# Performance work log

Measured on AMD Instinct MI355X. Metric: run time of the kernel, lower is better.

The kernel has to match this reference:

```python
import jax, jax.numpy as jnp
import numpy as np
from jax.scipy.special import logsumexp

# Special-tag indices (module-level globals in the original repo)
PAD_IDX, SOS_IDX, EOS_IDX = 0, 1, 2
NEG = -10000.0


def setup_inputs() -> dict:
    L, B, T = 1024, 2048, 16
    key = jax.random.key(0)
    k1, k2, k3, k4 = jax.random.split(key, 4)
    h = jax.random.normal(k1, (L, B, T), dtype=jnp.float32)
    y0 = jax.random.randint(k2, (L + 1, B), 0, T)  # gold tag path, [L+1, B]
    # prefix-of-ones mask from random lengths in [L//2, L]
    lengths = jax.random.randint(k4, (B,), L // 2, L + 1)
    mask = (jnp.arange(L)[:, None] < lengths[None, :]).astype(jnp.float32)
    # transition matrix, init as in CRF.__init__
    trans = jax.random.normal(k3, (T, T), dtype=jnp.float32) * 0.01
    trans = (trans.at[SOS_IDX, :].set(NEG)
                  .at[:, EOS_IDX].set(NEG)
                  .at[:, PAD_IDX].set(NEG)
                  .at[PAD_IDX, :].set(NEG)
                  .at[PAD_IDX, EOS_IDX].set(0.0)
                  .at[PAD_IDX, PAD_IDX].set(0.0))
    return {"h": h, "y0": y0, "mask": mask, "trans": trans}


def _crf_loss(h, y0, mask, trans):
    L, B, T = h.shape
    # ---- score(h, y0, mask): note original uses _emit = 0 (emissions unused here)
    # S[b] = sum_t trans[y0[t+1,b], y0[t,b]] * mask[t,b]  for t in [0, L-2]
    S = jnp.sum(trans[y0[1:L], y0[: L - 1]] * mask[: L - 1], axis=0)  # [B]
    lengths = jnp.sum(mask, axis=0).astype(jnp.int32)                  # [B]
    last_tag = y0[lengths, jnp.arange(B)]                              # [B]
    S = S + trans[PAD_IDX, last_tag]

    # ---- partition(h, mask): forward algorithm over sigmoid(h)
    hs = jax.nn.sigmoid(h)
    Z0 = jnp.full((B, T), NEG, dtype=h.dtype).at[:, SOS_IDX].set(0.0)

    def step(Z, xm):
        _h, _m = xm                                   # [B,T], [B]
        # _Z[b,i] = logsumexp_j( Z[b,j] + _h[b,i] + trans[i,j] )
        _Z = logsumexp(Z[:, None, :] + _h[:, :, None] + trans[None, :, :], axis=2)
        Z = _Z * _m[:, None] + Z * (1.0 - _m[:, None])
        return Z, None

    Z, _ = jax.lax.scan(step, Z0, (hs, mask))
    Z = logsumexp(Z + trans[EOS_IDX], axis=1)         # [B]

    return jnp.mean(Z - S)


def reference(h, y0, mask, trans):
    return _crf_loss(h, y0, mask, trans)
```

## Files before the change

kernel.cpp:

```cpp
#include <hip/hip_runtime.h>


typedef unsigned int u32;
typedef float f32x4 __attribute__((ext_vector_type(4)));
typedef short s16x4 __attribute__((ext_vector_type(4)));
typedef unsigned int u32x2 __attribute__((ext_vector_type(2)));

#define LOG2E 1.4426950408889634f
#define LN2   0.6931471805599453f
#define Bsz   2048
#define Lsz   1024
#define BT    32768

#if __has_builtin(__builtin_amdgcn_exp2f)
__device__ __forceinline__ float exp2x(float x){ return __builtin_amdgcn_exp2f(x); }
#else
__device__ __forceinline__ float exp2x(float x){ return exp2f(x); }
#endif
#if __has_builtin(__builtin_amdgcn_logf)
__device__ __forceinline__ float log2x(float x){ return __builtin_amdgcn_logf(x); }
#else
__device__ __forceinline__ float log2x(float x){ return log2f(x); }
#endif
#if __has_builtin(__builtin_amdgcn_rcpf)
__device__ __forceinline__ float rcpx(float x){ return __builtin_amdgcn_rcpf(x); }
#else
__device__ __forceinline__ float rcpx(float x){ return 1.0f/x; }
#endif

__device__ __forceinline__ u32 cvtpk_bf16(float lo, float hi){
  u32 r;
  asm("v_cvt_pk_bf16_f32 %0, %1, %2" : "=v"(r) : "v"(lo), "v"(hi));
  return r;
}

__device__ __forceinline__ f32x4 mfma16(s16x4 a, s16x4 b, f32x4 c){
  f32x4 d;
  asm volatile("s_nop 1\n\t"
      "v_mfma_f32_16x16x16_bf16 %0, %1, %2, %3\n\t"
      "s_nop 7\n\t"
      "s_nop 7"
      : "=&v"(d) : "v"(a), "v"(b), "v"(c));
  return d;
}

#define RUN_SEG(CNT, A0, A1, B0X, B0Y, B1X, B1Y, ELO, EHI)                     \
  asm volatile(                                                                \
    "s_waitcnt lgkmcnt(0)\n\t"                                                 \
    "v_mov_b32 v40, %[b0x]\n\t"                                                \
    "v_mov_b32 v41, %[b0y]\n\t"                                                \
    "v_mov_b32 v42, %[b1x]\n\t"                                                \
    "v_mov_b32 v43, %[b1y]\n\t"                                                \
    "v_mov_b32 v56, %[elo]\n\t"                                                \
    "v_mov_b32 v57, %[ehi]\n\t"                                                \
    "v_mov_b32 v58, 0\n\t"                                                     \
    "v_mov_b32 v59, 0\n\t"                                                     \
    "v_mov_b32 v60, 0\n\t"                                                     \
    "v_mov_b32 v61, 0\n\t"                                                     \
    ".LP%=:\n\t"                                                               \
    "ds_read_b128 v[44:47], %[a0]\n\t"                                         \
    "ds_read_b128 v[48:51], %[a1]\n\t"                                         \
    "v_add_u32 %[a0], 16, %[a0]\n\t"                                           \
    "v_add_u32 %[a1], 16, %[a1]\n\t"                                           \
    "s_waitcnt lgkmcnt(0)\n\t"                                                 \
    "s_nop 1\n\t"                                                              \
    "v_mfma_f32_16x16x16_bf16 v[32:35], v[56:57], v[40:41], v[58:61]\n\t"      \
    "v_mfma_f32_16x16x16_bf16 v[36:39], v[56:57], v[42:43], v[58:61]\n\t"      \
    "v_lshlrev_b32 v52, 16, v44\n\t"                                           \
    "v_and_b32 v53, 0xffff0000, v44\n\t"                                       \
    "v_lshlrev_b32 v54, 16, v45\n\t"                                           \
    "v_and_b32 v55, 0xffff0000, v45\n\t"                                       \
    "s_nop 6\n\t"                                                              \
    "v_mul_f32 v52, v32, v52\n\t"                                              \
    "v_mul_f32 v53, v33, v53\n\t"                                              \
    "v_mul_f32 v54, v34, v54\n\t"                                              \
    "v_mul_f32 v55, v35, v55\n\t"                                              \
    "v_cvt_pk_bf16_f32 v40, v52, v53\n\t"                                      \
    "v_cvt_pk_bf16_f32 v41, v54, v55\n\t"                                      \
    "v_lshlrev_b32 v52, 16, v48\n\t"                                           \
    "v_and_b32 v53, 0xffff0000, v48\n\t"                                       \
    "v_lshlrev_b32 v54, 16, v49\n\t"                                           \
    "v_and_b32 v55, 0xffff0000, v49\n\t"                                       \
    "v_mul_f32 v52, v36, v52\n\t"                                              \
    "v_mul_f32 v53, v37, v53\n\t"                                              \
    "v_mul_f32 v54, v38, v54\n\t"                                              \
    "v_mul_f32 v55, v39, v55\n\t"                                              \
    "v_cvt_pk_bf16_f32 v42, v52, v53\n\t"                                      \
    "v_cvt_pk_bf16_f32 v43, v54, v55\n\t"                                      \
    "s_nop 1\n\t"                                                              \
    "v_mfma_f32_16x16x16_bf16 v[32:35], v[56:57], v[40:41], v[58:61]\n\t"      \
    "v_mfma_f32_16x16x16_bf16 v[36:39], v[56:57], v[42:43], v[58:61]\n\t"      \
    "v_lshlrev_b32 v52, 16, v46\n\t"                                           \
    "v_and_b32 v53, 0xffff0000, v46\n\t"                                       \
    "v_lshlrev_b32 v54, 16, v47\n\t"                                           \
    "v_and_b32 v55, 0xffff0000, v47\n\t"                                       \
    "s_nop 6\n\t"                                                              \
    "v_mul_f32 v52, v32, v52\n\t"                                              \
    "v_mul_f32 v53, v33, v53\n\t"                                              \
    "v_mul_f32 v54, v34, v54\n\t"                                              \
    "v_mul_f32 v55, v35, v55\n\t"                                              \
    "v_cvt_pk_bf16_f32 v40, v52, v53\n\t"                                      \
    "v_cvt_pk_bf16_f32 v41, v54, v55\n\t"                                      \
    "v_lshlrev_b32 v52, 16, v50\n\t"                                           \
    "v_and_b32 v53, 0xffff0000, v50\n\t"                                       \
    "v_lshlrev_b32 v54, 16, v51\n\t"                                           \
    "v_and_b32 v55, 0xffff0000, v51\n\t"                                       \
    "v_mul_f32 v52, v36, v52\n\t"                                              \
    "v_mul_f32 v53, v37, v53\n\t"                                              \
    "v_mul_f32 v54, v38, v54\n\t"                                              \
    "v_mul_f32 v55, v39, v55\n\t"                                              \
    "v_cvt_pk_bf16_f32 v42, v52, v53\n\t"                                      \
    "v_cvt_pk_bf16_f32 v43, v54, v55\n\t"                                      \
    "s_sub_u32 %[cnt], %[cnt], 1\n\t"                                          \
    "s_cmp_lg_u32 %[cnt], 0\n\t"                                               \
    "s_cbranch_scc1 .LP%=\n\t"                                                 \
    "v_mov_b32 %[b0x], v40\n\t"                                                \
    "v_mov_b32 %[b0y], v41\n\t"                                                \
    "v_mov_b32 %[b1x], v42\n\t"                                                \
    "v_mov_b32 %[b1y], v43"                                                    \
    : [a0]"+v"(A0), [a1]"+v"(A1), [cnt]"+s"(CNT),                              \
      [b0x]"+v"(B0X), [b0y]"+v"(B0Y), [b1x]"+v"(B1X), [b1y]"+v"(B1Y)           \
    : [elo]"v"(ELO), [ehi]"v"(EHI)                                             \
    : "memory",                                                                \
      "v32","v33","v34","v35","v36","v37","v38","v39",                         \
      "v40","v41","v42","v43","v44","v45","v46","v47",                         \
      "v48","v49","v50","v51","v52","v53","v54","v55",                         \
      "v56","v57","v58","v59","v60","v61")

__global__ __launch_bounds__(256) void k_zero(float* lenw, float* Sw, float* out){
  int i = blockIdx.x*256 + threadIdx.x;
  if (i < Bsz) lenw[i] = 0.f;
  else if (i < 2*Bsz) Sw[i - Bsz] = 0.f;
  if (i == 0) out[0] = 0.f;
}

__global__ __launch_bounds__(256) void k_score(const int* __restrict__ y0,
    const float* __restrict__ mask, const float* __restrict__ trans,
    float* __restrict__ lenw, float* __restrict__ Sw){
  __shared__ float Tt[256];
  Tt[threadIdx.x] = trans[threadIdx.x];
  __syncthreads();
  int gid = blockIdx.x*256 + threadIdx.x;
  int b  = gid & (Bsz-1);
  int tc = gid >> 11;
  int t0 = tc * 32;
  float lacc = 0.f, sacc = 0.f;
  int yc = y0[t0*Bsz + b];
  #pragma unroll 4
  for (int t = t0; t < t0+32; ++t) {
    float m = mask[t*Bsz + b];
    int yn = y0[(t+1)*Bsz + b];
    lacc += m;
    if (t <= Lsz-2) sacc += m * Tt[yn*16 + yc];
    yc = yn;
  }
  atomicAdd(&lenw[b], lacc);
  atomicAdd(&Sw[b], sacc);
}

__global__ __launch_bounds__(256) void k_phase1(const float* __restrict__ h,
    const float* __restrict__ trans, const float* __restrict__ lenw,
    u32x2* __restrict__ Pout){
  __shared__ __align__(16) u32 gbuf[4][2][4*132];
  int warp = threadIdx.x >> 6;
  int wid  = blockIdx.x*4 + warp;
  int cpair= wid >> 11;
  int b    = wid & (Bsz-1);
  int lane = threadIdx.x & 63;
  int cl   = lane & 15;
  int grp  = lane >> 4;
  int len  = (int)(lenw[b] + 0.5f);
  int t0a  = cpair << 6;
  int t0b  = 512 + (cpair << 6);
  int a1   = len - t0b;
  a1 = a1 < 0 ? 0 : (a1 > 64 ? 64 : a1);

  {
    int m = lane & 7, trow = lane >> 3;
    #pragma unroll
    for (int cc = 0; cc < 2; ++cc) {
      if (cc == 1 && a1 <= 0) break;
      int tt0 = cc ? t0b : t0a;
      const float* hp = h + (size_t)tt0*BT + b*16 + 2*m;
      u32* wp = &gbuf[warp][cc][(m>>1)*132 + (m&1)];
      #pragma unroll
      for (int k = 0; k < 8; ++k) {
        int t = trow + 8*k;
        float2 hv = *(const float2*)&hp[(size_t)t*BT];
        float g0 = exp2x(rcpx(1.f + exp2x(hv.x * (-LOG2E))) * LOG2E);
        float g1 = exp2x(rcpx(1.f + exp2x(hv.y * (-LOG2E))) * LOG2E);
        wp[2*t] = cvtpk_bf16(g0, g1);
      }
    }
  }

  u32 elo, ehi;
  {
    const float* tp = trans + cl*16 + grp*4;
    float E0 = exp2x(tp[0]*LOG2E) * 0.0625f;
    float E1 = exp2x(tp[1]*LOG2E) * 0.0625f;
    float E2 = exp2x(tp[2]*LOG2E) * 0.0625f;
    float E3 = exp2x(tp[3]*LOG2E) * 0.0625f;
    elo = cvtpk_bf16(E0, E1);
    ehi = cvtpk_bf16(E2, E3);
  }

  int k0 = grp*4;
  u32 ibx = ((k0+0)==cl ? 0x3F80u : 0u) | (((k0+1)==cl ? 0x3F80u : 0u) << 16);
  u32 iby = ((k0+2)==cl ? 0x3F80u : 0u) | (((k0+3)==cl ? 0x3F80u : 0u) << 16);
  u32 b0x = ibx, b0y = iby, b1x = ibx, b1y = iby;

  u32 a0 = (u32)(unsigned long long)&gbuf[warp][0][grp*132];
  u32 a1a= (u32)(unsigned long long)&gbuf[warp][1][grp*132];

  int p = a1 >> 1;
  int odd = a1 & 1;

  if (p > 0) {
    u32 cnt = (u32)__builtin_amdgcn_readfirstlane(p);
    RUN_SEG(cnt, a0, a1a, b0x, b0y, b1x, b1y, elo, ehi);
  }

  if (odd) {
    u32x2 gw = *(const u32x2*)&gbuf[warp][1][grp*132 + 4*p];
    float f0 = __uint_as_float(gw.x << 16);
    float f1 = __uint_as_float(gw.x & 0xffff0000u);
    float f2 = __uint_as_float(gw.y << 16);
    float f3 = __uint_as_float(gw.y & 0xffff0000u);
    union { u32 u[2]; s16x4 v; } EAv, Bf;
    EAv.u[0] = elo; EAv.u[1] = ehi;
    Bf.u[0] = b1x; Bf.u[1] = b1y;
    const f32x4 z4 = {0.f,0.f,0.f,0.f};
    f32x4 d = mfma16(EAv.v, Bf.v, z4);
    b1x = cvtpk_bf16(d.x*f0, d.y*f1);
    b1y = cvtpk_bf16(d.z*f2, d.w*f3);
  }
  u32 p1x = b1x, p1y = b1y;

  if (p < 32) {
    u32 cnt = (u32)__builtin_amdgcn_readfirstlane(32 - p);
    RUN_SEG(cnt, a0, a1a, b0x, b0y, b1x, b1y, elo, ehi);
  }

  Pout[(size_t)(b*16 + cpair)*64 + lane] = (u32x2){b0x, b0y};
  if (a1 > 0)
    Pout[(size_t)(b*16 + cpair + 8)*64 + lane] = (u32x2){p1x, p1y};
}

__global__ __launch_bounds__(256) void k_phase2(const u32x2* __restrict__ P,
    const float* __restrict__ trans, const float* __restrict__ lenw,
    const float* __restrict__ Sw, const int* __restrict__ y0,
    float* __restrict__ out){
  __shared__ float red[4];
  int b = blockIdx.x*4 + (threadIdx.x >> 6);
  int lane = threadIdx.x & 63;
  int cl = lane & 15, grp = lane >> 4;
  int len = (int)(lenw[b] + 0.5f);
  float v = (cl == 1) ? 1.f : 0.f;
  float lsc = 0.f;
  int nch = (len + 63) >> 6;
  const u32x2* Pb = P + (size_t)b*16*64;
  int srcaddr = (cl >> 2) << 6;
  int msel = cl & 3;
  for (int c = 0; c < nch; ++c) {
    u32x2 pw = Pb[c*64 + lane];
    float p0 = __uint_as_float(pw.x << 16);
    float p1 = __uint_as_float(pw.x & 0xffff0000u);
    float p2 = __uint_as_float(pw.y << 16);
    float p3 = __uint_as_float(pw.y & 0xffff0000u);
    float q0 = p0*v, q1 = p1*v, q2 = p2*v, q3 = p3*v;
    #pragma unroll
    for (int mk = 1; mk <= 8; mk <<= 1) {
      q0 += __shfl_xor(q0, mk);
      q1 += __shfl_xor(q1, mk);
      q2 += __shfl_xor(q2, mk);
      q3 += __shfl_xor(q3, mk);
    }
    float t0v = __int_as_float(__builtin_amdgcn_ds_bpermute(srcaddr, __float_as_int(q0)));
    float t1v = __int_as_float(__builtin_amdgcn_ds_bpermute(srcaddr, __float_as_int(q1)));
    float t2v = __int_as_float(__builtin_amdgcn_ds_bpermute(srcaddr, __float_as_int(q2)));
    float t3v = __int_as_float(__builtin_amdgcn_ds_bpermute(srcaddr, __float_as_int(q3)));
    float vn = (msel==0) ? t0v : (msel==1) ? t1v : (msel==2) ? t2v : t3v;
    float gm = fmaxf(fmaxf(q0,q1), fmaxf(q2,q3));
    gm = fmaxf(gm, __shfl_xor(gm, 16));
    gm = fmaxf(gm, __shfl_xor(gm, 32));
    int eb = (int)((__float_as_uint(gm) >> 23) & 0xff) - 127;
    float sc = __uint_as_float((u32)(127 - eb) << 23);
    v = vn * sc;
    lsc += (float)eb;
  }
  float eE = exp2x(trans[32 + cl] * LOG2E);
  float num = v * eE;
  num += __shfl_xor(num, 1);
  num += __shfl_xor(num, 2);
  num += __shfl_xor(num, 4);
  num += __shfl_xor(num, 8);
  if (lane == 0) {
    float Z = (log2x(num) + lsc + 4.f*(float)len) * LN2;
    int lastTag = y0[(size_t)len*Bsz + b];
    float Sb = Sw[b] + trans[lastTag];
    red[threadIdx.x >> 6] = (Z - Sb) * (1.f/(float)Bsz);
  }
  __syncthreads();
  if (threadIdx.x == 0) {
    atomicAdd(out, red[0] + red[1] + red[2] + red[3]);
  }
}

extern "C" void kernel_launch(void* const* d_in, const int* in_sizes, int n_in,
                              void* d_out, int out_size, void* d_ws, size_t ws_size,
                              hipStream_t stream) {
  const float* h     = (const float*)d_in[0];
  const int*   y0    = (const int*)d_in[1];
  const float* mask  = (const float*)d_in[2];
  const float* trans = (const float*)d_in[3];
  float* out  = (float*)d_out;
  float* lenw = (float*)d_ws;
  float* Sw   = lenw + Bsz;
  u32x2* P    = (u32x2*)((char*)d_ws + 16384);

  k_zero  <<<16,   256, 0, stream>>>(lenw, Sw, out);
  k_score <<<256,  256, 0, stream>>>(y0, mask, trans, lenw, Sw);
  k_phase1<<<4096, 256, 0, stream>>>(h, trans, lenw, P);
  k_phase2<<<512,  256, 0, stream>>>(P, trans, lenw, Sw, y0, out);
}
```

Measured before the change: 91.20 us.

## Regroup phase1 work: block per 16 batches and one chunk, skip inactive chunks

Phase1 blocks now cover 16 batch rows times one 64-step time chunk. Each block loads h cooperatively with float4 coalesced reads into padded shared memory, and each warp pairs two batch rows in the interleaved MFMA recurrence. Blocks whose chunk lies entirely past every row's length exit early, and rows stop at their own active length. The earlier scheme always ran two chunks per warp (one always full). The new one skips padded work and improves global load coalescing, at the cost of a block barrier and more branching for uneven row lengths.

```diff
diff --git a/kernel.cpp b/kernel.cpp
--- a/kernel.cpp
+++ b/kernel.cpp
@@ -11,6 +11,7 @@
 #define Bsz   2048
 #define Lsz   1024
 #define BT    32768
+#define BSTR  556
 
 #if __has_builtin(__builtin_amdgcn_exp2f)
 __device__ __forceinline__ float exp2x(float x){ return __builtin_amdgcn_exp2f(x); }
@@ -161,38 +162,42 @@
 __global__ __launch_bounds__(256) void k_phase1(const float* __restrict__ h,
     const float* __restrict__ trans, const float* __restrict__ lenw,
     u32x2* __restrict__ Pout){
-  __shared__ __align__(16) u32 gbuf[4][2][4*132];
+  __shared__ __align__(16) u32 gbuf[16*BSTR];
+  int bg   = blockIdx.x & 127;
+  int c    = blockIdx.x >> 7;
   int warp = threadIdx.x >> 6;
-  int wid  = blockIdx.x*4 + warp;
-  int cpair= wid >> 11;
-  int b    = wid & (Bsz-1);
   int lane = threadIdx.x & 63;
   int cl   = lane & 15;
   int grp  = lane >> 4;
-  int len  = (int)(lenw[b] + 0.5f);
-  int t0a  = cpair << 6;
-  int t0b  = 512 + (cpair << 6);
-  int a1   = len - t0b;
-  a1 = a1 < 0 ? 0 : (a1 > 64 ? 64 : a1);
+  int t0   = c << 6;
+  int gb0  = bg*16 + warp*4;
+
+  int act[4]; int any = 0;
+  #pragma unroll
+  for (int i = 0; i < 4; ++i) {
+    int a = (int)(lenw[gb0 + i] + 0.5f) - t0;
+    a = a < 0 ? 0 : (a > 64 ? 64 : a);
+    act[i] = a; any |= a;
+  }
+  if (!__syncthreads_or(any)) return;
 
   {
-    int m = lane & 7, trow = lane >> 3;
+    int bq = lane >> 2, q = lane & 3;
+    const float* hp = h + (size_t)t0*BT + bg*256 + 4*lane;
+    u32* wp = &gbuf[bq*BSTR + q*132];
     #pragma unroll
-    for (int cc = 0; cc < 2; ++cc) {
-      if (cc == 1 && a1 <= 0) break;
-      int tt0 = cc ? t0b : t0a;
-      const float* hp = h + (size_t)tt0*BT + b*16 + 2*m;
-      u32* wp = &gbuf[warp][cc][(m>>1)*132 + (m&1)];
-      #pragma unroll
-      for (int k = 0; k < 8; ++k) {
-        int t = trow + 8*k;
-        float2 hv = *(const float2*)&hp[(size_t)t*BT];
-        float g0 = exp2x(rcpx(1.f + exp2x(hv.x * (-LOG2E))) * LOG2E);
-        float g1 = exp2x(rcpx(1.f + exp2x(hv.y * (-LOG2E))) * LOG2E);
-        wp[2*t] = cvtpk_bf16(g0, g1);
-      }
-    }
-  }
+    for (int i = 0; i < 16; ++i) {
+      int t = 4*i + warp;
+      const float4 hv = *(const float4*)(hp + (size_t)t*BT);
+      float g0 = exp2x(rcpx(1.f + exp2x(hv.x * (-LOG2E))) * LOG2E);
+      float g1 = exp2x(rcpx(1.f + exp2x(hv.y * (-LOG2E))) * LOG2E);
+      float g2 = exp2x(rcpx(1.f + exp2x(hv.z * (-LOG2E))) * LOG2E);
+      float g3 = exp2x(rcpx(1.f + exp2x(hv.w * (-LOG2E))) * LOG2E);
+      u32x2 pk; pk.x = cvtpk_bf16(g0, g1); pk.y = cvtpk_bf16(g2, g3);
+      *(u32x2*)&wp[2*t] = pk;
+    }
+  }
+  __syncthreads();
 
   u32 elo, ehi;
   {
@@ -204,47 +209,72 @@
     elo = cvtpk_bf16(E0, E1);
     ehi = cvtpk_bf16(E2, E3);
   }
-
   int k0 = grp*4;
-  u32 ibx = ((k0+0)==cl ? 0x3F80u : 0u) | (((k0+1)==cl ? 0x3F80u : 0u) << 16);
-  u32 iby = ((k0+2)==cl ? 0x3F80u : 0u) | (((k0+3)==cl ? 0x3F80u : 0u) << 16);
-  u32 b0x = ibx, b0y = iby, b1x = ibx, b1y = iby;
-
-  u32 a0 = (u32)(unsigned long long)&gbuf[warp][0][grp*132];
-  u32 a1a= (u32)(unsigned long long)&gbuf[warp][1][grp*132];
-
-  int p = a1 >> 1;
-  int odd = a1 & 1;
-
-  if (p > 0) {
-    u32 cnt = (u32)__builtin_amdgcn_readfirstlane(p);
-    RUN_SEG(cnt, a0, a1a, b0x, b0y, b1x, b1y, elo, ehi);
-  }
-
-  if (odd) {
-    u32x2 gw = *(const u32x2*)&gbuf[warp][1][grp*132 + 4*p];
-    float f0 = __uint_as_float(gw.x << 16);
-    float f1 = __uint_as_float(gw.x & 0xffff0000u);
-    float f2 = __uint_as_float(gw.y << 16);
-    float f3 = __uint_as_float(gw.y & 0xffff0000u);
-    union { u32 u[2]; s16x4 v; } EAv, Bf;
-    EAv.u[0] = elo; EAv.u[1] = ehi;
-    Bf.u[0] = b1x; Bf.u[1] = b1y;
-    const f32x4 z4 = {0.f,0.f,0.f,0.f};
-    f32x4 d = mfma16(EAv.v, Bf.v, z4);
-    b1x = cvtpk_bf16(d.x*f0, d.y*f1);
-    b1y = cvtpk_bf16(d.z*f2, d.w*f3);
-  }
-  u32 p1x = b1x, p1y = b1y;
-
-  if (p < 32) {
-    u32 cnt = (u32)__builtin_amdgcn_readfirstlane(32 - p);
-    RUN_SEG(cnt, a0, a1a, b0x, b0y, b1x, b1y, elo, ehi);
-  }
-
-  Pout[(size_t)(b*16 + cpair)*64 + lane] = (u32x2){b0x, b0y};
-  if (a1 > 0)
-    Pout[(size_t)(b*16 + cpair + 8)*64 + lane] = (u32x2){p1x, p1y};
+  const u32 ibx = ((k0+0)==cl ? 0x3F80u : 0u) | (((k0+1)==cl ? 0x3F80u : 0u) << 16);
+  const u32 iby = ((k0+2)==cl ? 0x3F80u : 0u) | (((k0+3)==cl ? 0x3F80u : 0u) << 16);
+  const f32x4 z4 = {0.f,0.f,0.f,0.f};
+
+  #define STEP1(BX, BY, GB, T) do {                                        \
+    u32x2 gw = *(const u32x2*)&(GB)[2*(T)];                                \
+    float f0 = __uint_as_float(gw.x << 16);                                \
+    float f1 = __uint_as_float(gw.x & 0xffff0000u);                        \
+    float f2 = __uint_as_float(gw.y << 16);                                \
+    float f3 = __uint_as_float(gw.y & 0xffff0000u);                        \
+    union { u32 u[2]; s16x4 v; } EAv, Bf;                                  \
+    EAv.u[0] = elo; EAv.u[1] = ehi;                                        \
+    Bf.u[0] = (BX); Bf.u[1] = (BY);                                        \
+    f32x4 d = mfma16(EAv.v, Bf.v, z4);                                     \
+    (BX) = cvtpk_bf16(d.x*f0, d.y*f1);                                     \
+    (BY) = cvtpk_bf16(d.z*f2, d.w*f3);                                     \
+  } while (0)
+
+  #pragma unroll
+  for (int pr = 0; pr < 2; ++pr) {
+    int iA = 2*pr, iB = 2*pr + 1;
+    int rA = act[iA], rB = act[iB];
+    if ((rA | rB) == 0) continue;
+    u32* gbA = &gbuf[(warp*4 + iA)*BSTR + grp*132];
+    u32* gbB = &gbuf[(warp*4 + iB)*BSTR + grp*132];
+    u32 aA = (u32)(unsigned long long)gbA;
+    u32 aB = (u32)(unsigned long long)gbB;
+    u32 bAx = ibx, bAy = iby, bBx = ibx, bBy = iby;
+    int m = rA < rB ? rA : rB;
+    int M = rA < rB ? rB : rA;
+    int p1 = m >> 1;
+    if (p1 > 0) {
+      u32 cnt = (u32)__builtin_amdgcn_readfirstlane(p1);
+      RUN_SEG(cnt, aA, aB, bAx, bAy, bBx, bBy, elo, ehi);
+    }
+    int te = 2*p1;
+    if (m & 1) {
+      if (rA == m) STEP1(bAx, bAy, gbA, te);
+      if (rB == m) STEP1(bBx, bBy, gbB, te);
+    }
+    if (rA == m && rA > 0)
+      Pout[((size_t)(gb0 + iA)*16 + c)*64 + lane] = (u32x2){bAx, bAy};
+    if (rB == m && rB > 0)
+      Pout[((size_t)(gb0 + iB)*16 + c)*64 + lane] = (u32x2){bBx, bBy};
+    if (M > m) {
+      int rem = M - te;
+      int p2 = rem >> 1;
+      if (rA > rB) {
+        if (p2 > 0) {
+          u32 cnt = (u32)__builtin_amdgcn_readfirstlane(p2);
+          RUN_SEG(cnt, aA, aB, bAx, bAy, bBx, bBy, elo, ehi);
+        }
+        if (rem & 1) STEP1(bAx, bAy, gbA, te + 2*p2);
+        Pout[((size_t)(gb0 + iA)*16 + c)*64 + lane] = (u32x2){bAx, bAy};
+      } else {
+        if (p2 > 0) {
+          u32 cnt = (u32)__builtin_amdgcn_readfirstlane(p2);
+          RUN_SEG(cnt, aB, aA, bBx, bBy, bAx, bAy, elo, ehi);
+        }
+        if (rem & 1) STEP1(bBx, bBy, gbB, te + 2*p2);
+        Pout[((size_t)(gb0 + iB)*16 + c)*64 + lane] = (u32x2){bBx, bBy};
+      }
+    }
+  }
+  #undef STEP1
 }
 
 __global__ __launch_bounds__(256) void k_phase2(const u32x2* __restrict__ P,
@@ -321,6 +351,6 @@
 
   k_zero  <<<16,   256, 0, stream>>>(lenw, Sw, out);
   k_score <<<256,  256, 0, stream>>>(y0, mask, trans, lenw, Sw);
-  k_phase1<<<4096, 256, 0, stream>>>(h, trans, lenw, P);
+  k_phase1<<<2048, 256, 0, stream>>>(h, trans, lenw, P);
   k_phase2<<<512,  256, 0, stream>>>(P, trans, lenw, Sw, y0, out);
 }
```

Result: slower. 96.49 us (+5.8%).
